# Performance work log

Hardware: AMD Instinct MI355X
Metric: run time of the kernel (lower is better)

The kernel has to match this reference:

```python
import jax, jax.numpy as jnp
import numpy as np

VOLRADIUS = 256.0
DT = 1.0 / VOLRADIUS  # self.dt = dt / volradius with dt=1.0
N_STEPS = 64
B, H, W, K, M = 1, 256, 256, 64, 16


def setup_inputs() -> dict:
    rng = np.random.default_rng(0)
    # orthographic-ish ray bundle looking down +z through the primitive cloud
    ys, xs = np.meshgrid(np.linspace(-1., 1., H, dtype=np.float32),
                         np.linspace(-1., 1., W, dtype=np.float32), indexing='ij')
    raypos = np.broadcast_to(np.stack([xs, ys, np.full_like(xs, -0.125)], -1)[None],
                             (B, H, W, 3)).astype(np.float32).copy()
    raydir = np.zeros((B, H, W, 3), np.float32); raydir[..., 2] = 1.0
    tmin = np.zeros((B, H, W), np.float32)
    tminmax = np.stack([tmin, tmin + N_STEPS * DT], -1).astype(np.float32)
    # primpos is in WORLD units (module divides by volradius)
    primpos = rng.uniform(-0.1 * VOLRADIUS, 0.1 * VOLRADIUS, (B, K, 3)).astype(np.float32)
    q, _ = np.linalg.qr(rng.normal(size=(B, K, 3, 3)))
    primrot = q.astype(np.float32)
    primscale = rng.uniform(8., 16., (B, K, 3)).astype(np.float32)  # inverse half-extent
    primrgba = rng.uniform(0., 1., (B, K, 4, M, M, M)).astype(np.float32)
    return {
        'raypos': jnp.asarray(raypos), 'raydir': jnp.asarray(raydir),
        'tminmax': jnp.asarray(tminmax), 'primpos': jnp.asarray(primpos),
        'primrot': jnp.asarray(primrot), 'primscale': jnproundtrip(primscale) if False else jnp.asarray(primscale),
        'primrgba': jnp.asarray(primrgba),
    }


def _trilinear_sum(template, pos, primpos, primrot, primscale):
    # template [K,4,M,M,M]; pos [R,3]; returns summed rgba over primitives [R,4]
    Mv = template.shape[-1]
    kidx = jnp.arange(template.shape[0])[None, :]                      # [1,K]
    rel = pos[:, None, :] - primpos[None, :, :]                        # [R,K,3]
    # local = primscale * (primrot^T @ rel), inside prim iff |local| < 1
    local = jnp.einsum('kij,rki->rkj', primrot, rel) * primscale[None]  # [R,K,3]
    inside = jnp.all(jnp.abs(local) < 1.0, axis=-1)                    # [R,K]
    g = jnp.clip((local + 1.0) * 0.5 * (Mv - 1), 0.0, Mv - 1 - 1e-5)    # voxel coords (x,y,z)
    i0 = jnp.clip(jnp.floor(g).astype(jnp.int32), 0, Mv - 2)
    f = g - i0.astype(g.dtype)
    x0, y0, z0 = i0[..., 0], i0[..., 1], i0[..., 2]
    fx, fy, fz = f[..., 0], f[..., 1], f[..., 2]
    c = jnp.zeros(local.shape[:2] + (4,), template.dtype)
    for dz, wz in ((0, 1 - fz), (1, fz)):
        for dy, wy in ((0, 1 - fy), (1, fy)):
            for dx, wx in ((0, 1 - fx), (1, fx)):
                corner = template[kidx, :, z0 + dz, y0 + dy, x0 + dx]  # [R,K,4]
                c = c + corner * (wz * wy * wx)[..., None]
    c = c * inside[..., None]
    return c.sum(axis=1)                                               # [R,4]


def _march(raypos, raydir, tminmax, primpos, primrot, primscale, template):
    Hh, Ww, _ = raypos.shape
    R = Hh * Ww
    o = raypos.reshape(R, 3)
    d = raydir.reshape(R, 3)
    tmm = tminmax.reshape(R, 2)
    tmin, tmax = tmm[:, 0], tmm[:, 1]

    def step(carry, i):
        rgb, alpha = carry
        t = tmin + (i.astype(jnp.float32) + 0.5) * DT
        valid = t < tmax
        pos = o + t[:, None] * d
        s = _trilinear_sum(template, pos, primpos, primrot, primscale)  # [R,4]
        # MVP front-to-back saturating alpha compositing (early-term equivalent)
        contrib = jnp.minimum(1.0, alpha + s[:, 3] * DT) - alpha
        contrib = jnp.where(valid, contrib, 0.0)
        rgb = rgb + s[:, :3] * contrib[:, None]
        alpha = alpha + contrib
        return (rgb, alpha), None

    init = (jnp.zeros((R, 3), jnp.float32), jnp.zeros((R,), jnp.float32))
    (rgb, alpha), _ = jax.lax.scan(jax.checkpoint(step), init, jnp.arange(N_STEPS))
    return jnp.concatenate([rgb, alpha[:, None]], -1).reshape(Hh, Ww, 4)


def reference(raypos, raydir, tminmax, primpos, primrot, primscale, primrgba):
    primpos_n = primpos / VOLRADIUS  # module normalizes primpos by volume radius
    rayrgba = jax.vmap(_march)(raypos, raydir, tminmax, primpos_n, primrot, primscale, primrgba)
    rayrgba = jnp.transpose(rayrgba, (0, 3, 1, 2))  # [B,4,H,W]
    rayrgb = rayrgba[:, :3]
    rayalpha = rayrgba[:, 3:4]
    return rayrgb, rayalpha, rayrgba
```

## Files before the change

kernel.cpp:

```cpp
#include <hip/hip_runtime.h>
#include <hip/hip_fp16.h>

#define Rtot 65536
#define Wimg 256
#define Kp 64
#define NSTEPS 64
#define DTc (1.0f/256.0f)
#define INV_VOLR (1.0f/256.0f)
#define NITEMS 16384

#define PD_OFF    0u
#define TB_OFF    4096u
#define FLAG_OFF  20480u
#define TT_OFF    65536u
#define SBUF_OFF  8388608u
#define WS_NEED   (SBUF_OFF + (size_t)NITEMS*256*8)

typedef _Float16 half2v __attribute__((ext_vector_type(2)));

__device__ __forceinline__ half2v u2h(unsigned int u) {
  union { unsigned int u; half2v h; } x; x.u = u; return x.h;
}
__device__ __forceinline__ half2v mkh2(float a, float b) {
  half2v h; h.x = (_Float16)a; h.y = (_Float16)b; return h;
}
__device__ __forceinline__ unsigned int pack2(float a, float b) {
  __half2 h = __floats2half2_rn(a, b);
  return *(unsigned int*)&h;
}

#if __has_builtin(__builtin_amdgcn_fdot2)
#define FDOT2(a, b, c) __builtin_amdgcn_fdot2((a), (b), (c), false)
#else
#define FDOT2(a, b, c) ((float)(a).x*(float)(b).x + (float)(a).y*(float)(b).y + (c))
#endif

__global__ __launch_bounds__(256) void setup_kernel(
    const float* __restrict__ raypos, const float* __restrict__ raydir,
    const float* __restrict__ tminmax, const float* __restrict__ primpos,
    const float* __restrict__ primrot, const float* __restrict__ primscale,
    const float* __restrict__ tmpl,
    float* __restrict__ tb, uint4* __restrict__ tth, float* __restrict__ pd) {
  int bid = blockIdx.x, tid = threadIdx.x;
  if (bid < 256) {
    __shared__ float smn[4][7], smx[4][7];
    int w = (bid & 15)*16 + (tid & 15);
    int h = (bid >> 4)*16 + (tid >> 4);
    int r = h*Wimg + w;
    float v[7];
    v[0] = raypos[r*3+0]; v[1] = raypos[r*3+1]; v[2] = raypos[r*3+2];
    v[3] = raydir[r*3+0]; v[4] = raydir[r*3+1]; v[5] = raydir[r*3+2];
    v[6] = tminmax[r*2+0];
    float mn[7], mx[7];
#pragma unroll
    for (int i = 0; i < 7; ++i) { mn[i] = v[i]; mx[i] = v[i]; }
#pragma unroll
    for (int m = 1; m < 64; m <<= 1) {
#pragma unroll
      for (int i = 0; i < 7; ++i) {
        mn[i] = fminf(mn[i], __shfl_xor(mn[i], m));
        mx[i] = fmaxf(mx[i], __shfl_xor(mx[i], m));
      }
    }
    int wv = tid >> 6;
    if ((tid & 63) == 0) {
#pragma unroll
      for (int i = 0; i < 7; ++i) { smn[wv][i] = mn[i]; smx[wv][i] = mx[i]; }
    }
    __syncthreads();
    if (tid == 0) {
#pragma unroll
      for (int i = 0; i < 7; ++i) {
        tb[bid*16 + i]     = fminf(fminf(smn[0][i], smn[1][i]), fminf(smn[2][i], smn[3][i]));
        tb[bid*16 + 8 + i] = fmaxf(fmaxf(smx[0][i], smx[1][i]), fmaxf(smx[2][i], smx[3][i]));
      }
    }
  } else if (bid < 512) {
    int k = (bid - 256) >> 2;
    int q = (bid - 256) & 3;
    const float* b0 = tmpl + (((size_t)k) << 14);
    uint4* o = tth + (k << 12);
#pragma unroll
    for (int s = 0; s < 4; ++s) {
      int v = q*1024 + s*256 + tid;
      int x = v & 15;
      int xn = (x < 15) ? v + 1 : v;
      uint4 qq;
      qq.x = pack2(b0[v],       b0[xn]);
      qq.y = pack2(b0[4096+v],  b0[4096+xn]);
      qq.z = pack2(b0[8192+v],  b0[8192+xn]);
      qq.w = pack2(b0[12288+v], b0[12288+xn]);
      o[v] = qq;
    }
  } else {
    int k = tid;
    if (k < Kp) {
      float sc0 = primscale[k*3+0], sc1 = primscale[k*3+1], sc2 = primscale[k*3+2];
      float* o = pd + (k << 4);
      o[0] = primpos[k*3+0] * INV_VOLR;
      o[1] = primpos[k*3+1] * INV_VOLR;
      o[2] = primpos[k*3+2] * INV_VOLR;
      o[3] = 0.0f; o[4] = 0.0f; o[5] = 0.0f;
#pragma unroll
      for (int i = 0; i < 3; ++i) {
        o[6+i*3+0] = primrot[k*9+i*3+0]*sc0;
        o[6+i*3+1] = primrot[k*9+i*3+1]*sc1;
        o[6+i*3+2] = primrot[k*9+i*3+2]*sc2;
      }
      o[15] = 0.0f;
    }
  }
}

__global__ __launch_bounds__(256) void shade_kernel(
    const float* __restrict__ raypos, const float* __restrict__ raydir,
    const float* __restrict__ tminmax, const float* __restrict__ pd,
    const float* __restrict__ tb, const uint4* __restrict__ tth,
    unsigned long long* __restrict__ sbuf, unsigned char* __restrict__ flags) {
  __shared__ int s_list[Kp];
  __shared__ int s_cnt;
  int item = blockIdx.x;
  int tile = item >> 6, step = item & 63;
  int tid = threadIdx.x;
  if (tid < 64) {
    const float* t0 = tb + tile*16;
    float cst = ((float)step + 0.5f)*DTc;
    float tl = t0[6] + cst, th = t0[14] + cst;
    const float* p = pd + (tid << 4);
    float rlo[3], rhi[3];
#pragma unroll
    for (int a = 0; a < 3; ++a) {
      float ol = t0[a], oh = t0[8+a], dl = t0[3+a], dh = t0[11+a];
      float p1 = tl*dl, p2 = tl*dh, p3 = th*dl, p4 = th*dh;
      rlo[a] = ol + fminf(fminf(p1, p2), fminf(p3, p4)) - p[a];
      rhi[a] = oh + fmaxf(fmaxf(p1, p2), fmaxf(p3, p4)) - p[a];
    }
    bool pass = true;
#pragma unroll
    for (int j = 0; j < 3; ++j) {
      float llo = 0.f, lhi = 0.f;
#pragma unroll
      for (int a = 0; a < 3; ++a) {
        float rsc = p[6+a*3+j];
        float q1 = rlo[a]*rsc, q2 = rhi[a]*rsc;
        llo += fminf(q1, q2);
        lhi += fmaxf(q1, q2);
      }
      pass = pass && (llo < 1.0f) && (lhi > -1.0f);
    }
    unsigned long long mask = __ballot(pass);
    if (tid == 0) s_cnt = (int)__popcll(mask);
    if (pass) {
      int pos = (int)__popcll(mask & ((1ull << tid) - 1ull));
      s_list[pos] = tid;
    }
  }
  __syncthreads();
  int cnt = s_cnt;
  if (tid == 0) flags[item] = (unsigned char)(cnt > 0 ? 1 : 0);
  if (cnt == 0) return;

  int w = (tile & 15)*16 + (tid & 15);
  int h = (tile >> 4)*16 + (tid >> 4);
  int r = h*Wimg + w;
  float t = tminmax[r*2] + ((float)step + 0.5f)*DTc;
  float px = fmaf(t, raydir[r*3+0], raypos[r*3+0]);
  float py = fmaf(t, raydir[r*3+1], raypos[r*3+1]);
  float pz = fmaf(t, raydir[r*3+2], raypos[r*3+2]);
  float c0 = 0.f, c1 = 0.f, c2 = 0.f, c3 = 0.f;

  for (int j = 0; j < cnt; ++j) {
    int k = __builtin_amdgcn_readfirstlane(s_list[j]);
    const float* p = pd + (k << 4);
    float relx = px - p[0], rely = py - p[1], relz = pz - p[2];
    float lx = relx*p[6] + rely*p[9]  + relz*p[12];
    float ly = relx*p[7] + rely*p[10] + relz*p[13];
    float lz = relx*p[8] + rely*p[11] + relz*p[14];
    bool inside = fabsf(lx) < 1.0f && fabsf(ly) < 1.0f && fabsf(lz) < 1.0f;
    if (!__any(inside)) continue;
    if (inside) {
      float gx = fminf(fmaxf((lx + 1.0f)*7.5f, 0.0f), 14.99999f);
      float gy = fminf(fmaxf((ly + 1.0f)*7.5f, 0.0f), 14.99999f);
      float gz = fminf(fmaxf((lz + 1.0f)*7.5f, 0.0f), 14.99999f);
      int ix = (int)gx, iy = (int)gy, iz = (int)gz;
      float fx = gx - (float)ix, fy = gy - (float)iy, fz = gz - (float)iz;
      float wx0 = 1.0f - fx;
      float wy0 = 1.0f - fy, wz0 = 1.0f - fz;
      float w00 = wz0*wy0, w01 = wz0*fy, w10 = fz*wy0, w11 = fz*fy;
      const uint4* a = tth + ((size_t)k << 12) + (iz*256 + iy*16 + ix);
      uint4 q0 = a[0], q1 = a[16], q2 = a[256], q3 = a[272];
      half2v wp0 = mkh2(w00*wx0, w00*fx);
      half2v wp1 = mkh2(w01*wx0, w01*fx);
      half2v wp2 = mkh2(w10*wx0, w10*fx);
      half2v wp3 = mkh2(w11*wx0, w11*fx);
      c0 = FDOT2(u2h(q0.x), wp0, c0);
      c1 = FDOT2(u2h(q0.y), wp0, c1);
      c2 = FDOT2(u2h(q0.z), wp0, c2);
      c3 = FDOT2(u2h(q0.w), wp0, c3);
      c0 = FDOT2(u2h(q1.x), wp1, c0);
      c1 = FDOT2(u2h(q1.y), wp1, c1);
      c2 = FDOT2(u2h(q1.z), wp1, c2);
      c3 = FDOT2(u2h(q1.w), wp1, c3);
      c0 = FDOT2(u2h(q2.x), wp2, c0);
      c1 = FDOT2(u2h(q2.y), wp2, c1);
      c2 = FDOT2(u2h(q2.z), wp2, c2);
      c3 = FDOT2(u2h(q2.w), wp2, c3);
      c0 = FDOT2(u2h(q3.x), wp3, c0);
      c1 = FDOT2(u2h(q3.y), wp3, c1);
      c2 = FDOT2(u2h(q3.z), wp3, c2);
      c3 = FDOT2(u2h(q3.w), wp3, c3);
    }
  }
  unsigned long long pk = ((unsigned long long)pack2(c2, c3) << 32)
                        | (unsigned long long)pack2(c0, c1);
  sbuf[item*256 + tid] = pk;
}

__global__ __launch_bounds__(256) void composite_kernel(
    const float* __restrict__ tminmax, const unsigned long long* __restrict__ sbuf,
    const unsigned char* __restrict__ flags, float* __restrict__ out) {
  __shared__ unsigned char s_flags[NSTEPS];
  int tid = threadIdx.x;
  int b = blockIdx.x;
  if (tid < NSTEPS) s_flags[tid] = flags[b*NSTEPS + tid];
  __syncthreads();
  int w = (b & 15)*16 + (tid & 15);
  int h = (b >> 4)*16 + (tid >> 4);
  int r = h*Wimg + w;
  float tmin = tminmax[r*2+0], tmax = tminmax[r*2+1];
  float rgb0 = 0.f, rgb1 = 0.f, rgb2 = 0.f, alpha = 0.f;
  for (int i = 0; i < NSTEPS; ++i) {
    float s0 = 0.f, s1 = 0.f, s2 = 0.f, s3 = 0.f;
    if (s_flags[i]) {
      unsigned long long pk = sbuf[(b*NSTEPS + i)*256 + tid];
      unsigned int lo = (unsigned int)pk, hi = (unsigned int)(pk >> 32);
      float2 lf = __half22float2(*(__half2*)&lo);
      float2 hf = __half22float2(*(__half2*)&hi);
      s0 = lf.x; s1 = lf.y; s2 = hf.x; s3 = hf.y;
    }
    float t = tmin + ((float)i + 0.5f)*DTc;
    float contrib = fminf(1.0f, fmaf(s3, DTc, alpha)) - alpha;
    contrib = (t < tmax) ? contrib : 0.0f;
    rgb0 = fmaf(s0, contrib, rgb0);
    rgb1 = fmaf(s1, contrib, rgb1);
    rgb2 = fmaf(s2, contrib, rgb2);
    alpha += contrib;
  }
  out[0*Rtot + r] = rgb0;
  out[1*Rtot + r] = rgb1;
  out[2*Rtot + r] = rgb2;
  out[3*Rtot + r] = alpha;
  out[4*Rtot + r] = rgb0;
  out[5*Rtot + r] = rgb1;
  out[6*Rtot + r] = rgb2;
  out[7*Rtot + r] = alpha;
}

__global__ __launch_bounds__(256) void fallback_kernel(
    const float* __restrict__ raypos, const float* __restrict__ raydir,
    const float* __restrict__ tminmax,
    const float* __restrict__ primpos, const float* __restrict__ primrot,
    const float* __restrict__ primscale, const float* __restrict__ tmpl,
    float* __restrict__ out) {
  __shared__ float s_pd[Kp][16];
  int tx = threadIdx.x, ty = threadIdx.y;
  int tid = ty*16 + tx;
  if (tid < Kp) {
    int k = tid;
    float sc0 = primscale[k*3+0], sc1 = primscale[k*3+1], sc2 = primscale[k*3+2];
    s_pd[k][0] = primpos[k*3+0]*INV_VOLR;
    s_pd[k][1] = primpos[k*3+1]*INV_VOLR;
    s_pd[k][2] = primpos[k*3+2]*INV_VOLR;
#pragma unroll
    for (int i = 0; i < 3; ++i) {
      s_pd[k][6+i*3+0] = primrot[k*9+i*3+0]*sc0;
      s_pd[k][6+i*3+1] = primrot[k*9+i*3+1]*sc1;
      s_pd[k][6+i*3+2] = primrot[k*9+i*3+2]*sc2;
    }
  }
  __syncthreads();
  int w = blockIdx.x*16 + tx, h = blockIdx.y*16 + ty;
  int r = h*Wimg + w;
  float ox = raypos[r*3+0], oy = raypos[r*3+1], oz = raypos[r*3+2];
  float dx = raydir[r*3+0], dy = raydir[r*3+1], dz = raydir[r*3+2];
  float tmin = tminmax[r*2+0], tmax = tminmax[r*2+1];
  float rgb0=0.f, rgb1=0.f, rgb2=0.f, alpha=0.f;
  for (int i = 0; i < NSTEPS; ++i) {
    float t = tmin + ((float)i + 0.5f)*DTc;
    float px = fmaf(t, dx, ox), py = fmaf(t, dy, oy), pz = fmaf(t, dz, oz);
    float c[4] = {0.f, 0.f, 0.f, 0.f};
    for (int k = 0; k < Kp; ++k) {
      const float* p = &s_pd[k][0];
      float relx = px - p[0], rely = py - p[1], relz = pz - p[2];
      float lx = relx*p[6] + rely*p[9]  + relz*p[12];
      float ly = relx*p[7] + rely*p[10] + relz*p[13];
      float lz = relx*p[8] + rely*p[11] + relz*p[14];
      if (!(fabsf(lx) < 1.0f && fabsf(ly) < 1.0f && fabsf(lz) < 1.0f)) continue;
      float gx = fminf(fmaxf((lx + 1.0f)*7.5f, 0.0f), 14.99999f);
      float gy = fminf(fmaxf((ly + 1.0f)*7.5f, 0.0f), 14.99999f);
      float gz = fminf(fmaxf((lz + 1.0f)*7.5f, 0.0f), 14.99999f);
      int ix = (int)gx, iy = (int)gy, iz = (int)gz;
      ix = ix > 14 ? 14 : ix; iy = iy > 14 ? 14 : iy; iz = iz > 14 ? 14 : iz;
      float fx = gx - (float)ix, fy = gy - (float)iy, fz = gz - (float)iz;
      float wx0 = 1.0f - fx, wy0 = 1.0f - fy, wz0 = 1.0f - fz;
      float w00 = wz0*wy0, w01 = wz0*fy, w10 = fz*wy0, w11 = fz*fy;
      const float* base = tmpl + (((size_t)k) << 14) + iz*256 + iy*16 + ix;
#pragma unroll
      for (int ch = 0; ch < 4; ++ch) {
        const float* bb = base + ch*4096;
        c[ch] += (bb[0]  *wx0 + bb[1]  *fx) * w00
               + (bb[16] *wx0 + bb[17] *fx) * w01
               + (bb[256]*wx0 + bb[257]*fx) * w10
               + (bb[272]*wx0 + bb[273]*fx) * w11;
      }
    }
    float contrib = fminf(1.0f, fmaf(c[3], DTc, alpha)) - alpha;
    contrib = (t < tmax) ? contrib : 0.0f;
    rgb0 = fmaf(c[0], contrib, rgb0);
    rgb1 = fmaf(c[1], contrib, rgb1);
    rgb2 = fmaf(c[2], contrib, rgb2);
    alpha += contrib;
  }
  out[0*Rtot + r] = rgb0;
  out[1*Rtot + r] = rgb1;
  out[2*Rtot + r] = rgb2;
  out[3*Rtot + r] = alpha;
  out[4*Rtot + r] = rgb0;
  out[5*Rtot + r] = rgb1;
  out[6*Rtot + r] = rgb2;
  out[7*Rtot + r] = alpha;
}

extern "C" void kernel_launch(void* const* d_in, const int* in_sizes, int n_in,
                              void* d_out, int out_size, void* d_ws, size_t ws_size,
                              hipStream_t stream) {
  const float* raypos    = (const float*)d_in[0];
  const float* raydir    = (const float*)d_in[1];
  const float* tminmax   = (const float*)d_in[2];
  const float* primpos   = (const float*)d_in[3];
  const float* primrot   = (const float*)d_in[4];
  const float* primscale = (const float*)d_in[5];
  const float* primrgba  = (const float*)d_in[6];
  float* out = (float*)d_out;

  if (ws_size >= WS_NEED) {
    char* ws = (char*)d_ws;
    float* pd            = (float*)(ws + PD_OFF);
    float* tb            = (float*)(ws + TB_OFF);
    unsigned char* flags = (unsigned char*)(ws + FLAG_OFF);
    uint4* tth           = (uint4*)(ws + TT_OFF);
    unsigned long long* sbuf = (unsigned long long*)(ws + SBUF_OFF);

    setup_kernel<<<513, 256, 0, stream>>>(raypos, raydir, tminmax, primpos,
                                          primrot, primscale, primrgba,
                                          tb, tth, pd);
    shade_kernel<<<NITEMS, 256, 0, stream>>>(raypos, raydir, tminmax, pd, tb,
                                             tth, sbuf, flags);
    composite_kernel<<<256, 256, 0, stream>>>(tminmax, sbuf, flags, out);
  } else {
    fallback_kernel<<<dim3(16,16), dim3(16,16), 0, stream>>>(
        raypos, raydir, tminmax, primpos, primrot, primscale, primrgba, out);
  }
}
```

Before: 67.60 us.

## Software-pipeline primitive gathers with branchless double-buffered loads and LDS-staged params

```diff
diff --git a/kernel.cpp b/kernel.cpp
--- a/kernel.cpp
+++ b/kernel.cpp
@@ -112,21 +112,70 @@
   }
 }
 
+#define PSET(S, kk, vm)                                                      \
+  { const float* p = s_pd + ((kk) << 4);                                     \
+    float relx = px - p[0], rely = py - p[1], relz = pz - p[2];              \
+    float lx = relx*p[6] + rely*p[9]  + relz*p[12];                          \
+    float ly = relx*p[7] + rely*p[10] + relz*p[13];                          \
+    float lz = relx*p[8] + rely*p[11] + relz*p[14];                          \
+    bool inside = fabsf(lx) < 1.0f && fabsf(ly) < 1.0f && fabsf(lz) < 1.0f;  \
+    float gx = fminf(fmaxf((lx + 1.0f)*7.5f, 0.0f), 14.99999f);              \
+    float gy = fminf(fmaxf((ly + 1.0f)*7.5f, 0.0f), 14.99999f);              \
+    float gz = fminf(fmaxf((lz + 1.0f)*7.5f, 0.0f), 14.99999f);              \
+    int ix = (int)gx, iy = (int)gy, iz = (int)gz;                            \
+    float fx = gx - (float)ix, fy = gy - (float)iy, fz = gz - (float)iz;     \
+    float m = inside ? (vm) : 0.0f;                                          \
+    int idx = iz*256 + iy*16 + ix;                                           \
+    idx = inside ? idx : 0;                                                  \
+    float wy0 = 1.0f - fy, wz0m = (1.0f - fz)*m, fzm = fz*m;                 \
+    float wx0 = 1.0f - fx;                                                   \
+    float w00 = wz0m*wy0, w01 = wz0m*fy, w10 = fzm*wy0, w11 = fzm*fy;        \
+    w0##S = mkh2(w00*wx0, w00*fx);                                           \
+    w1##S = mkh2(w01*wx0, w01*fx);                                           \
+    w2##S = mkh2(w10*wx0, w10*fx);                                           \
+    w3##S = mkh2(w11*wx0, w11*fx);                                           \
+    const uint4* a = tth + ((size_t)(kk) << 12) + idx;                       \
+    q0##S = a[0]; q1##S = a[16]; q2##S = a[256]; q3##S = a[272]; }
+
+#define PACC(S)                                                              \
+  { c0 = FDOT2(u2h(q0##S.x), w0##S, c0);                                     \
+    c1 = FDOT2(u2h(q0##S.y), w0##S, c1);                                     \
+    c2 = FDOT2(u2h(q0##S.z), w0##S, c2);                                     \
+    c3 = FDOT2(u2h(q0##S.w), w0##S, c3);                                     \
+    c0 = FDOT2(u2h(q1##S.x), w1##S, c0);                                     \
+    c1 = FDOT2(u2h(q1##S.y), w1##S, c1);                                     \
+    c2 = FDOT2(u2h(q1##S.z), w1##S, c2);                                     \
+    c3 = FDOT2(u2h(q1##S.w), w1##S, c3);                                     \
+    c0 = FDOT2(u2h(q2##S.x), w2##S, c0);                                     \
+    c1 = FDOT2(u2h(q2##S.y), w2##S, c1);                                     \
+    c2 = FDOT2(u2h(q2##S.z), w2##S, c2);                                     \
+    c3 = FDOT2(u2h(q2##S.w), w2##S, c3);                                     \
+    c0 = FDOT2(u2h(q3##S.x), w3##S, c0);                                     \
+    c1 = FDOT2(u2h(q3##S.y), w3##S, c1);                                     \
+    c2 = FDOT2(u2h(q3##S.z), w3##S, c2);                                     \
+    c3 = FDOT2(u2h(q3##S.w), w3##S, c3); }
+
 __global__ __launch_bounds__(256) void shade_kernel(
     const float* __restrict__ raypos, const float* __restrict__ raydir,
     const float* __restrict__ tminmax, const float* __restrict__ pd,
     const float* __restrict__ tb, const uint4* __restrict__ tth,
     unsigned long long* __restrict__ sbuf, unsigned char* __restrict__ flags) {
-  __shared__ int s_list[Kp];
+  __shared__ float s_pd[Kp*16];
+  __shared__ int s_list[Kp + 1];
   __shared__ int s_cnt;
   int item = blockIdx.x;
   int tile = item >> 6, step = item & 63;
   int tid = threadIdx.x;
+  {
+    const float4* src = (const float4*)pd;
+    ((float4*)s_pd)[tid] = src[tid];
+  }
+  __syncthreads();
   if (tid < 64) {
     const float* t0 = tb + tile*16;
     float cst = ((float)step + 0.5f)*DTc;
     float tl = t0[6] + cst, th = t0[14] + cst;
-    const float* p = pd + (tid << 4);
+    const float* p = s_pd + (tid << 4);
     float rlo[3], rhi[3];
 #pragma unroll
     for (int a = 0; a < 3; ++a) {
@@ -149,7 +198,11 @@
       pass = pass && (llo < 1.0f) && (lhi > -1.0f);
     }
     unsigned long long mask = __ballot(pass);
-    if (tid == 0) s_cnt = (int)__popcll(mask);
+    int cnt = (int)__popcll(mask);
+    if (tid == 0) {
+      s_cnt = cnt;
+      if (cnt & 1) s_list[cnt] = (int)(__ffsll((long long)mask) - 1);
+    }
     if (pass) {
       int pos = (int)__popcll(mask & ((1ull << tid) - 1ull));
       s_list[pos] = tid;
@@ -159,6 +212,7 @@
   int cnt = s_cnt;
   if (tid == 0) flags[item] = (unsigned char)(cnt > 0 ? 1 : 0);
   if (cnt == 0) return;
+  int cntp = (cnt + 1) & ~1;
 
   int w = (tile & 15)*16 + (tid & 15);
   int h = (tile >> 4)*16 + (tid >> 4);
@@ -169,48 +223,25 @@
   float pz = fmaf(t, raydir[r*3+2], raypos[r*3+2]);
   float c0 = 0.f, c1 = 0.f, c2 = 0.f, c3 = 0.f;
 
-  for (int j = 0; j < cnt; ++j) {
-    int k = __builtin_amdgcn_readfirstlane(s_list[j]);
-    const float* p = pd + (k << 4);
-    float relx = px - p[0], rely = py - p[1], relz = pz - p[2];
-    float lx = relx*p[6] + rely*p[9]  + relz*p[12];
-    float ly = relx*p[7] + rely*p[10] + relz*p[13];
-    float lz = relx*p[8] + rely*p[11] + relz*p[14];
-    bool inside = fabsf(lx) < 1.0f && fabsf(ly) < 1.0f && fabsf(lz) < 1.0f;
-    if (!__any(inside)) continue;
-    if (inside) {
-      float gx = fminf(fmaxf((lx + 1.0f)*7.5f, 0.0f), 14.99999f);
-      float gy = fminf(fmaxf((ly + 1.0f)*7.5f, 0.0f), 14.99999f);
-      float gz = fminf(fmaxf((lz + 1.0f)*7.5f, 0.0f), 14.99999f);
-      int ix = (int)gx, iy = (int)gy, iz = (int)gz;
-      float fx = gx - (float)ix, fy = gy - (float)iy, fz = gz - (float)iz;
-      float wx0 = 1.0f - fx;
-      float wy0 = 1.0f - fy, wz0 = 1.0f - fz;
-      float w00 = wz0*wy0, w01 = wz0*fy, w10 = fz*wy0, w11 = fz*fy;
-      const uint4* a = tth + ((size_t)k << 12) + (iz*256 + iy*16 + ix);
-      uint4 q0 = a[0], q1 = a[16], q2 = a[256], q3 = a[272];
-      half2v wp0 = mkh2(w00*wx0, w00*fx);
-      half2v wp1 = mkh2(w01*wx0, w01*fx);
-      half2v wp2 = mkh2(w10*wx0, w10*fx);
-      half2v wp3 = mkh2(w11*wx0, w11*fx);
-      c0 = FDOT2(u2h(q0.x), wp0, c0);
-      c1 = FDOT2(u2h(q0.y), wp0, c1);
-      c2 = FDOT2(u2h(q0.z), wp0, c2);
-      c3 = FDOT2(u2h(q0.w), wp0, c3);
-      c0 = FDOT2(u2h(q1.x), wp1, c0);
-      c1 = FDOT2(u2h(q1.y), wp1, c1);
-      c2 = FDOT2(u2h(q1.z), wp1, c2);
-      c3 = FDOT2(u2h(q1.w), wp1, c3);
-      c0 = FDOT2(u2h(q2.x), wp2, c0);
-      c1 = FDOT2(u2h(q2.y), wp2, c1);
-      c2 = FDOT2(u2h(q2.z), wp2, c2);
-      c3 = FDOT2(u2h(q2.w), wp2, c3);
-      c0 = FDOT2(u2h(q3.x), wp3, c0);
-      c1 = FDOT2(u2h(q3.y), wp3, c1);
-      c2 = FDOT2(u2h(q3.z), wp3, c2);
-      c3 = FDOT2(u2h(q3.w), wp3, c3);
-    }
-  }
+  uint4 q0A, q1A, q2A, q3A, q0B, q1B, q2B, q3B;
+  half2v w0A, w1A, w2A, w3A, w0B, w1B, w2B, w3B;
+
+  int kk = __builtin_amdgcn_readfirstlane(s_list[0]);
+  PSET(A, kk, 1.0f)
+  int j = 1;
+  for (; j < cntp - 1; j += 2) {
+    kk = __builtin_amdgcn_readfirstlane(s_list[j]);
+    PSET(B, kk, (j < cnt) ? 1.0f : 0.0f)
+    PACC(A)
+    kk = __builtin_amdgcn_readfirstlane(s_list[j+1]);
+    PSET(A, kk, (j+1 < cnt) ? 1.0f : 0.0f)
+    PACC(B)
+  }
+  kk = __builtin_amdgcn_readfirstlane(s_list[cntp-1]);
+  PSET(B, kk, (cntp-1 < cnt) ? 1.0f : 0.0f)
+  PACC(A)
+  PACC(B)
+
   unsigned long long pk = ((unsigned long long)pack2(c2, c3) << 32)
                         | (unsigned long long)pack2(c0, c1);
   sbuf[item*256 + tid] = pk;
```

Result: slower. 70.30 us (+4.0%).

## Process four march steps per shade block with incremental local coordinates

Applied to the files above, without the earlier changes.

```diff
diff --git a/kernel.cpp b/kernel.cpp
--- a/kernel.cpp
+++ b/kernel.cpp
@@ -7,14 +7,14 @@
 #define NSTEPS 64
 #define DTc (1.0f/256.0f)
 #define INV_VOLR (1.0f/256.0f)
-#define NITEMS 16384
+#define NITEMS2 4096
 
 #define PD_OFF    0u
 #define TB_OFF    4096u
 #define FLAG_OFF  20480u
 #define TT_OFF    65536u
 #define SBUF_OFF  8388608u
-#define WS_NEED   (SBUF_OFF + (size_t)NITEMS*256*8)
+#define WS_NEED   (SBUF_OFF + (size_t)16384*256*8)
 
 typedef _Float16 half2v __attribute__((ext_vector_type(2)));
 
@@ -112,6 +112,38 @@
   }
 }
 
+#define TRI_ACC(lx, ly, lz, cc0, cc1, cc2, cc3) {                            \
+    float gx = fminf(fmaxf(((lx) + 1.0f)*7.5f, 0.0f), 14.99999f);            \
+    float gy = fminf(fmaxf(((ly) + 1.0f)*7.5f, 0.0f), 14.99999f);            \
+    float gz = fminf(fmaxf(((lz) + 1.0f)*7.5f, 0.0f), 14.99999f);            \
+    int ix = (int)gx, iy = (int)gy, iz = (int)gz;                            \
+    float fx = gx - (float)ix, fy = gy - (float)iy, fz = gz - (float)iz;     \
+    float wx0 = 1.0f - fx;                                                   \
+    float wy0 = 1.0f - fy, wz0 = 1.0f - fz;                                  \
+    float w00 = wz0*wy0, w01 = wz0*fy, w10 = fz*wy0, w11 = fz*fy;            \
+    const uint4* a = tbase + (iz*256 + iy*16 + ix);                          \
+    uint4 q0 = a[0], q1 = a[16], q2 = a[256], q3 = a[272];                   \
+    half2v wp0 = mkh2(w00*wx0, w00*fx);                                      \
+    half2v wp1 = mkh2(w01*wx0, w01*fx);                                      \
+    half2v wp2 = mkh2(w10*wx0, w10*fx);                                      \
+    half2v wp3 = mkh2(w11*wx0, w11*fx);                                      \
+    cc0 = FDOT2(u2h(q0.x), wp0, cc0);                                        \
+    cc1 = FDOT2(u2h(q0.y), wp0, cc1);                                        \
+    cc2 = FDOT2(u2h(q0.z), wp0, cc2);                                        \
+    cc3 = FDOT2(u2h(q0.w), wp0, cc3);                                        \
+    cc0 = FDOT2(u2h(q1.x), wp1, cc0);                                        \
+    cc1 = FDOT2(u2h(q1.y), wp1, cc1);                                        \
+    cc2 = FDOT2(u2h(q1.z), wp1, cc2);                                        \
+    cc3 = FDOT2(u2h(q1.w), wp1, cc3);                                        \
+    cc0 = FDOT2(u2h(q2.x), wp2, cc0);                                        \
+    cc1 = FDOT2(u2h(q2.y), wp2, cc1);                                        \
+    cc2 = FDOT2(u2h(q2.z), wp2, cc2);                                        \
+    cc3 = FDOT2(u2h(q2.w), wp2, cc3);                                        \
+    cc0 = FDOT2(u2h(q3.x), wp3, cc0);                                        \
+    cc1 = FDOT2(u2h(q3.y), wp3, cc1);                                        \
+    cc2 = FDOT2(u2h(q3.z), wp3, cc2);                                        \
+    cc3 = FDOT2(u2h(q3.w), wp3, cc3); }
+
 __global__ __launch_bounds__(256) void shade_kernel(
     const float* __restrict__ raypos, const float* __restrict__ raydir,
     const float* __restrict__ tminmax, const float* __restrict__ pd,
@@ -120,12 +152,12 @@
   __shared__ int s_list[Kp];
   __shared__ int s_cnt;
   int item = blockIdx.x;
-  int tile = item >> 6, step = item & 63;
+  int tile = item >> 4, sg = item & 15;
   int tid = threadIdx.x;
   if (tid < 64) {
     const float* t0 = tb + tile*16;
-    float cst = ((float)step + 0.5f)*DTc;
-    float tl = t0[6] + cst, th = t0[14] + cst;
+    float tl = t0[6]  + ((float)(sg*4) + 0.5f)*DTc;
+    float th = t0[14] + ((float)(sg*4) + 3.5f)*DTc;
     const float* p = pd + (tid << 4);
     float rlo[3], rhi[3];
 #pragma unroll
@@ -163,88 +195,80 @@
   int w = (tile & 15)*16 + (tid & 15);
   int h = (tile >> 4)*16 + (tid >> 4);
   int r = h*Wimg + w;
-  float t = tminmax[r*2] + ((float)step + 0.5f)*DTc;
-  float px = fmaf(t, raydir[r*3+0], raypos[r*3+0]);
-  float py = fmaf(t, raydir[r*3+1], raypos[r*3+1]);
-  float pz = fmaf(t, raydir[r*3+2], raypos[r*3+2]);
-  float c0 = 0.f, c1 = 0.f, c2 = 0.f, c3 = 0.f;
+  float ox = raypos[r*3+0], oy = raypos[r*3+1], oz = raypos[r*3+2];
+  float dx = raydir[r*3+0], dy = raydir[r*3+1], dz = raydir[r*3+2];
+  float t0s = tminmax[r*2] + ((float)(sg*4) + 0.5f)*DTc;
+
+  float c00=0.f,c01=0.f,c02=0.f,c03=0.f;
+  float c10=0.f,c11=0.f,c12=0.f,c13=0.f;
+  float c20=0.f,c21=0.f,c22=0.f,c23=0.f;
+  float c30=0.f,c31=0.f,c32=0.f,c33=0.f;
 
   for (int j = 0; j < cnt; ++j) {
     int k = __builtin_amdgcn_readfirstlane(s_list[j]);
     const float* p = pd + (k << 4);
-    float relx = px - p[0], rely = py - p[1], relz = pz - p[2];
-    float lx = relx*p[6] + rely*p[9]  + relz*p[12];
-    float ly = relx*p[7] + rely*p[10] + relz*p[13];
-    float lz = relx*p[8] + rely*p[11] + relz*p[14];
-    bool inside = fabsf(lx) < 1.0f && fabsf(ly) < 1.0f && fabsf(lz) < 1.0f;
-    if (!__any(inside)) continue;
-    if (inside) {
-      float gx = fminf(fmaxf((lx + 1.0f)*7.5f, 0.0f), 14.99999f);
-      float gy = fminf(fmaxf((ly + 1.0f)*7.5f, 0.0f), 14.99999f);
-      float gz = fminf(fmaxf((lz + 1.0f)*7.5f, 0.0f), 14.99999f);
-      int ix = (int)gx, iy = (int)gy, iz = (int)gz;
-      float fx = gx - (float)ix, fy = gy - (float)iy, fz = gz - (float)iz;
-      float wx0 = 1.0f - fx;
-      float wy0 = 1.0f - fy, wz0 = 1.0f - fz;
-      float w00 = wz0*wy0, w01 = wz0*fy, w10 = fz*wy0, w11 = fz*fy;
-      const uint4* a = tth + ((size_t)k << 12) + (iz*256 + iy*16 + ix);
-      uint4 q0 = a[0], q1 = a[16], q2 = a[256], q3 = a[272];
-      half2v wp0 = mkh2(w00*wx0, w00*fx);
-      half2v wp1 = mkh2(w01*wx0, w01*fx);
-      half2v wp2 = mkh2(w10*wx0, w10*fx);
-      half2v wp3 = mkh2(w11*wx0, w11*fx);
-      c0 = FDOT2(u2h(q0.x), wp0, c0);
-      c1 = FDOT2(u2h(q0.y), wp0, c1);
-      c2 = FDOT2(u2h(q0.z), wp0, c2);
-      c3 = FDOT2(u2h(q0.w), wp0, c3);
-      c0 = FDOT2(u2h(q1.x), wp1, c0);
-      c1 = FDOT2(u2h(q1.y), wp1, c1);
-      c2 = FDOT2(u2h(q1.z), wp1, c2);
-      c3 = FDOT2(u2h(q1.w), wp1, c3);
-      c0 = FDOT2(u2h(q2.x), wp2, c0);
-      c1 = FDOT2(u2h(q2.y), wp2, c1);
-      c2 = FDOT2(u2h(q2.z), wp2, c2);
-      c3 = FDOT2(u2h(q2.w), wp2, c3);
-      c0 = FDOT2(u2h(q3.x), wp3, c0);
-      c1 = FDOT2(u2h(q3.y), wp3, c1);
-      c2 = FDOT2(u2h(q3.z), wp3, c2);
-      c3 = FDOT2(u2h(q3.w), wp3, c3);
-    }
-  }
-  unsigned long long pk = ((unsigned long long)pack2(c2, c3) << 32)
-                        | (unsigned long long)pack2(c0, c1);
-  sbuf[item*256 + tid] = pk;
+    float rox = ox - p[0], roy = oy - p[1], roz = oz - p[2];
+    float Ax = rox*p[6] + roy*p[9]  + roz*p[12];
+    float Ay = rox*p[7] + roy*p[10] + roz*p[13];
+    float Az = rox*p[8] + roy*p[11] + roz*p[14];
+    float Bx = dx*p[6] + dy*p[9]  + dz*p[12];
+    float By = dx*p[7] + dy*p[10] + dz*p[13];
+    float Bz = dx*p[8] + dy*p[11] + dz*p[14];
+    float l0x = fmaf(t0s, Bx, Ax), l0y = fmaf(t0s, By, Ay), l0z = fmaf(t0s, Bz, Az);
+    float dbx = Bx*DTc, dby = By*DTc, dbz = Bz*DTc;
+    float l1x = l0x + dbx, l1y = l0y + dby, l1z = l0z + dbz;
+    float l2x = l1x + dbx, l2y = l1y + dby, l2z = l1z + dbz;
+    float l3x = l2x + dbx, l3y = l2y + dby, l3z = l2z + dbz;
+    bool in0 = fabsf(l0x) < 1.0f && fabsf(l0y) < 1.0f && fabsf(l0z) < 1.0f;
+    bool in1 = fabsf(l1x) < 1.0f && fabsf(l1y) < 1.0f && fabsf(l1z) < 1.0f;
+    bool in2 = fabsf(l2x) < 1.0f && fabsf(l2y) < 1.0f && fabsf(l2z) < 1.0f;
+    bool in3 = fabsf(l3x) < 1.0f && fabsf(l3y) < 1.0f && fabsf(l3z) < 1.0f;
+    if (!__any(in0 || in1 || in2 || in3)) continue;
+    const uint4* tbase = tth + ((size_t)k << 12);
+    if (in0) TRI_ACC(l0x, l0y, l0z, c00, c01, c02, c03)
+    if (in1) TRI_ACC(l1x, l1y, l1z, c10, c11, c12, c13)
+    if (in2) TRI_ACC(l2x, l2y, l2z, c20, c21, c22, c23)
+    if (in3) TRI_ACC(l3x, l3y, l3z, c30, c31, c32, c33)
+  }
+  int base = (tile*NSTEPS + sg*4)*256 + tid;
+  sbuf[base +   0] = ((unsigned long long)pack2(c02, c03) << 32) | pack2(c00, c01);
+  sbuf[base + 256] = ((unsigned long long)pack2(c12, c13) << 32) | pack2(c10, c11);
+  sbuf[base + 512] = ((unsigned long long)pack2(c22, c23) << 32) | pack2(c20, c21);
+  sbuf[base + 768] = ((unsigned long long)pack2(c32, c33) << 32) | pack2(c30, c31);
 }
 
 __global__ __launch_bounds__(256) void composite_kernel(
     const float* __restrict__ tminmax, const unsigned long long* __restrict__ sbuf,
     const unsigned char* __restrict__ flags, float* __restrict__ out) {
-  __shared__ unsigned char s_flags[NSTEPS];
+  __shared__ unsigned char s_flags[16];
   int tid = threadIdx.x;
   int b = blockIdx.x;
-  if (tid < NSTEPS) s_flags[tid] = flags[b*NSTEPS + tid];
+  if (tid < 16) s_flags[tid] = flags[b*16 + tid];
   __syncthreads();
   int w = (b & 15)*16 + (tid & 15);
   int h = (b >> 4)*16 + (tid >> 4);
   int r = h*Wimg + w;
   float tmin = tminmax[r*2+0], tmax = tminmax[r*2+1];
   float rgb0 = 0.f, rgb1 = 0.f, rgb2 = 0.f, alpha = 0.f;
-  for (int i = 0; i < NSTEPS; ++i) {
-    float s0 = 0.f, s1 = 0.f, s2 = 0.f, s3 = 0.f;
-    if (s_flags[i]) {
-      unsigned long long pk = sbuf[(b*NSTEPS + i)*256 + tid];
-      unsigned int lo = (unsigned int)pk, hi = (unsigned int)(pk >> 32);
-      float2 lf = __half22float2(*(__half2*)&lo);
-      float2 hf = __half22float2(*(__half2*)&hi);
-      s0 = lf.x; s1 = lf.y; s2 = hf.x; s3 = hf.y;
-    }
-    float t = tmin + ((float)i + 0.5f)*DTc;
-    float contrib = fminf(1.0f, fmaf(s3, DTc, alpha)) - alpha;
-    contrib = (t < tmax) ? contrib : 0.0f;
-    rgb0 = fmaf(s0, contrib, rgb0);
-    rgb1 = fmaf(s1, contrib, rgb1);
-    rgb2 = fmaf(s2, contrib, rgb2);
-    alpha += contrib;
+  for (int g = 0; g < 16; ++g) {
+    if (s_flags[g]) {
+#pragma unroll
+      for (int i4 = 0; i4 < 4; ++i4) {
+        int i = g*4 + i4;
+        unsigned long long pk = sbuf[(b*NSTEPS + i)*256 + tid];
+        unsigned int lo = (unsigned int)pk, hi = (unsigned int)(pk >> 32);
+        float2 lf = __half22float2(*(__half2*)&lo);
+        float2 hf = __half22float2(*(__half2*)&hi);
+        float t = tmin + ((float)i + 0.5f)*DTc;
+        float contrib = fminf(1.0f, fmaf(hf.y, DTc, alpha)) - alpha;
+        contrib = (t < tmax) ? contrib : 0.0f;
+        rgb0 = fmaf(lf.x, contrib, rgb0);
+        rgb1 = fmaf(lf.y, contrib, rgb1);
+        rgb2 = fmaf(hf.x, contrib, rgb2);
+        alpha += contrib;
+      }
+    } else {
+    }
   }
   out[0*Rtot + r] = rgb0;
   out[1*Rtot + r] = rgb1;
@@ -354,8 +378,8 @@
     setup_kernel<<<513, 256, 0, stream>>>(raypos, raydir, tminmax, primpos,
                                           primrot, primscale, primrgba,
                                           tb, tth, pd);
-    shade_kernel<<<NITEMS, 256, 0, stream>>>(raypos, raydir, tminmax, pd, tb,
-                                             tth, sbuf, flags);
+    shade_kernel<<<NITEMS2, 256, 0, stream>>>(raypos, raydir, tminmax, pd, tb,
+                                              tth, sbuf, flags);
     composite_kernel<<<256, 256, 0, stream>>>(tminmax, sbuf, flags, out);
   } else {
     fallback_kernel<<<dim3(16,16), dim3(16,16), 0, stream>>>(
```

After: 104.4 us. 1.54x slower.
